# Performance work log

Measured on AMD Instinct MI355X. Metric: run time of the kernel, lower is better.

The kernel has to match this reference:

```python
import jax, jax.numpy as jnp
import numpy as np

N_NODES = 100_000
N_EDGES = 1_600_000
F_IN = 128
HID = 64
C_OUT = 16


def setup_inputs() -> dict:
    key = jax.random.key(0)
    k1, k2, k3, k4, k5 = jax.random.split(key, 5)
    x = jax.random.normal(k1, (N_NODES, F_IN), dtype=jnp.float32)
    edge_index = jax.random.randint(k2, (2, N_EDGES), 0, N_NODES, dtype=jnp.int64)
    edge_weight = jax.random.uniform(k3, (N_EDGES,), dtype=jnp.float32)
    # Glorot-ish init for the two GCNConv linear layers; PyG inits bias to zero.
    W1 = jax.random.normal(k4, (F_IN, HID), dtype=jnp.float32) * (1.0 / np.sqrt(F_IN))
    b1 = jnp.zeros((HID,), dtype=jnp.float32)
    W2 = jax.random.normal(k5, (HID, C_OUT), dtype=jnp.float32) * (1.0 / np.sqrt(HID))
    b2 = jnp.zeros((C_OUT,), dtype=jnp.float32)
    return {"x": x, "edge_index": edge_index, "edge_weight": edge_weight,
            "W1": W1, "b1": b1, "W2": W2, "b2": b2}


def gcn_layer(x, row, col, ew, W, b, n):
    """PyG GCNConv: h = D^-1/2 (A + I) D^-1/2 (x W) + b, with edge weights.
    Self loops (weight 1) are handled analytically instead of appending edges."""
    h = x @ W  # [n, out]
    deg = jax.ops.segment_sum(ew, col, num_segments=n) + 1.0  # +1 for self loop
    dinv = jax.lax.rsqrt(deg)  # deg >= 1 always
    norm = dinv[row] * ew * dinv[col]  # [E]
    agg = jax.ops.segment_sum(norm[:, None] * h[row], col, num_segments=n)
    return agg + (dinv * dinv)[:, None] * h + b


def reference(x, edge_index, edge_weight, W1, b1, W2, b2):
    row, col = edge_index[0], edge_index[1]
    h = jax.nn.relu(gcn_layer(x, row, col, edge_weight, W1, b1, N_NODES))
    # delete_min_weighted_edges(node=0): remove the min-weight edge with source 0.
    # Zeroing its weight is mathematically identical to deleting it (it then
    # contributes 0 to both the degree and the aggregation).
    masked = jnp.where(row == 0, edge_weight, jnp.inf)
    idx = jnp.argmin(masked)
    ew2 = edge_weight.at[idx].set(0.0)
    return gcn_layer(h, row, col, ew2, W2, b2, N_NODES)
```

## Files before the change

### kernel.cpp

```cpp
#include <hip/hip_runtime.h>
#include <hip/hip_bf16.h>
#include <stdint.h>

#define NN 100000
#define NE 1600000
#define FIN 128
#define HID 64
#define COUT 16

#define BUKSH 8
#define BUKN 256
#define NBUK ((NN + BUKN - 1) >> BUKSH)
#define CAP 5120
#define PART_NB 200
#define EPB (NE / PART_NB)

typedef unsigned long long u64;
typedef short bf16x8 __attribute__((ext_vector_type(8)));
typedef float f32x4 __attribute__((ext_vector_type(4)));

struct Flags { int f32; int i64; };

__device__ __forceinline__ float b2f(__hip_bfloat16 v) { return __bfloat162float(v); }

__device__ __forceinline__ float ldf(const void* p, size_t i, int f32) {
    return f32 ? ((const float*)p)[i]
               : __bfloat162float(((const __hip_bfloat16*)p)[i]);
}
__device__ __forceinline__ int lde(const void* p, size_t i, int i64) {
    return i64 ? (int)((const long long*)p)[i] : ((const int*)p)[i];
}
__device__ __forceinline__ void ld4bf(const __hip_bfloat16* p, float& x0, float& x1,
                                      float& x2, float& x3) {
    union { uint2 u; __hip_bfloat16 h[4]; } v;
    v.u = *(const uint2*)p;
    x0 = b2f(v.h[0]); x1 = b2f(v.h[1]); x2 = b2f(v.h[2]); x3 = b2f(v.h[3]);
}
__device__ __forceinline__ unsigned short f2bfu(float f) {
    union { __hip_bfloat16 b; unsigned short u; } c;
    c.b = __float2bfloat16(f);
    return c.u;
}
__device__ __forceinline__ float bfu2f(unsigned short u) {
    union { unsigned short h[2]; float f; } c;
    c.h[0] = 0; c.h[1] = u;
    return c.f;
}

__global__ void k_detect(const unsigned short* xs, const int* ei32, Flags* fl) {
    int lane = threadIdx.x & 63;
    int huge = 0;
    for (int i = lane * 2; i < 1024; i += 128) {
        int e = (xs[i] >> 7) & 0xFF;
        if (e >= 0xC0) huge = 1;
    }
    int odd_nonzero = 0;
    for (int i = 1 + lane * 2; i < 512; i += 128) {
        if (ei32[i] != 0) odd_nonzero = 1;
    }
    u64 h = __ballot(huge), o = __ballot(odd_nonzero);
    if (lane == 0) { fl->f32 = (h != 0); fl->i64 = (o == 0); }
}

__global__ void k_mink(const void* __restrict__ ei, const void* __restrict__ ew,
                       const Flags* __restrict__ fl, u64* __restrict__ minkey) {
    int e = blockIdx.x * blockDim.x + threadIdx.x;
    if (e >= NE) return;
    int r = lde(ei, e, fl->i64);
    if (r == 0) {
        float w = ldf(ew, e, fl->f32);
        u64 key = ((u64)__float_as_uint(w) << 32) | (unsigned)e;
        atomicMin(minkey, key);
    }
}

__global__ __launch_bounds__(256) void k_partA(const void* __restrict__ ei,
                                               const void* __restrict__ ew,
                                               const Flags* __restrict__ fl,
                                               const u64* __restrict__ minkey,
                                               int* __restrict__ cursorA,
                                               long long* __restrict__ tmp) {
    __shared__ int cnt[NBUK];
    __shared__ int base[NBUK];
    int b = blockIdx.x, t = threadIdx.x;
    int f32 = fl->f32, i64 = fl->i64;
    for (int i = t; i < NBUK; i += 256) cnt[i] = 0;
    __syncthreads();
    int e0 = b * EPB;
    for (int i = t; i < EPB; i += 256) {
        int c = lde(ei, (size_t)NE + e0 + i, i64);
        atomicAdd(&cnt[c >> BUKSH], 1);
    }
    __syncthreads();
    for (int i = t; i < NBUK; i += 256) {
        int n = cnt[i];
        base[i] = n ? atomicAdd(&cursorA[i], n) : 0;
    }
    __syncthreads();
    for (int i = t; i < NBUK; i += 256) cnt[i] = 0;
    __syncthreads();
    u64 k = *minkey;
    int eidx = (k == ~0ull) ? 0 : (int)(k & 0xffffffffu);
    for (int i = t; i < EPB; i += 256) {
        int e = e0 + i;
        int r = lde(ei, e, i64);
        int c = lde(ei, (size_t)NE + e, i64);
        float w = ldf(ew, e, f32);
        int buk = c >> BUKSH;
        int slot = base[buk] + atomicAdd(&cnt[buk], 1);
        if (slot < CAP) {
            unsigned lo = (unsigned)r | (((unsigned)c & 255u) << 17)
                        | ((e == eidx) ? (1u << 25) : 0u);
            tmp[(size_t)buk * CAP + slot] = ((long long)__float_as_int(w) << 32) | lo;
        }
    }
}

__global__ __launch_bounds__(512) void k_scanBk(const int* __restrict__ cursorA,
                                                int* __restrict__ bucketBase,
                                                int* __restrict__ rowptrN) {
    __shared__ int sm[512];
    int t = threadIdx.x;
    int v = 0;
    if (t < NBUK) { v = cursorA[t]; if (v > CAP) v = CAP; }
    sm[t] = v;
    for (int off = 1; off < 512; off <<= 1) {
        __syncthreads();
        int add = (t >= off) ? sm[t - off] : 0;
        __syncthreads();
        sm[t] += add;
    }
    __syncthreads();
    if (t < NBUK) bucketBase[t] = sm[t] - v;
    if (t == 511) rowptrN[NN] = sm[511];
}

__global__ __launch_bounds__(256) void k_partB(const int* __restrict__ cursorA,
                                               const int* __restrict__ bucketBase,
                                               const long long* __restrict__ tmp,
                                               int2* __restrict__ epack,
                                               int* __restrict__ rowptrN,
                                               const void* __restrict__ ei,
                                               const void* __restrict__ ew,
                                               const Flags* __restrict__ fl,
                                               const u64* __restrict__ minkey,
                                               float* __restrict__ dinv1,
                                               float* __restrict__ dinv2,
                                               int* __restrict__ delpos) {
    __shared__ int cnt[256];
    __shared__ int pfx[256];
    __shared__ u64 wsum[256];
    int b = blockIdx.x, t = threadIdx.x;
    cnt[t] = 0; wsum[t] = 0;
    __syncthreads();
    int count = cursorA[b]; if (count > CAP) count = CAP;
    const long long* ts = tmp + (size_t)b * CAP;
    for (int i = t; i < count; i += 256) {
        long long pk = ts[i];
        unsigned lo = (unsigned)pk;
        int nl = (int)((lo >> 17) & 255u);
        atomicAdd(&cnt[nl], 1);
        float w = __int_as_float((int)(pk >> 32));
        atomicAdd(&wsum[nl], (u64)((double)w * 4294967296.0));
    }
    __syncthreads();
    int v = cnt[t];
    pfx[t] = v;
    for (int off = 1; off < 256; off <<= 1) {
        __syncthreads();
        int add = (t >= off) ? pfx[t - off] : 0;
        __syncthreads();
        pfx[t] += add;
    }
    __syncthreads();
    int excl = pfx[t] - v;
    int gbase = bucketBase[b];
    int node = (b << BUKSH) + t;
    if (node < NN) {
        rowptrN[node] = gbase + excl;
        float degv = (float)((double)wsum[t] * (1.0 / 4294967296.0));
        u64 kk = *minkey;
        int eidx = (kk == ~0ull) ? 0 : (int)(kk & 0xffffffffu);
        int cmin = lde(ei, (size_t)NE + eidx, fl->i64);
        float wmin = ldf(ew, eidx, fl->f32);
        float d1 = degv + 1.0f;
        float d2 = d1 - ((node == cmin) ? wmin : 0.0f);
        dinv1[node] = rsqrtf(d1);
        dinv2[node] = rsqrtf(d2);
    }
    __syncthreads();
    cnt[t] = gbase + excl;
    __syncthreads();
    for (int i = t; i < count; i += 256) {
        long long pk = ts[i];
        unsigned lo = (unsigned)pk;
        int nl = (int)((lo >> 17) & 255u);
        int pos = atomicAdd(&cnt[nl], 1);
        long long outpk = (pk & 0xFFFFFFFF00000000LL) | (lo & 0x1FFFFu);
        *(long long*)(epack + pos) = outpk;
        if (lo & (1u << 25)) *delpos = pos;
    }
}

__global__ __launch_bounds__(256, 3) void k_gemm1_split(const float* __restrict__ x,
                                                        const float* __restrict__ W1,
                                                        const Flags* __restrict__ fl,
                                                        const float* __restrict__ dinv1,
                                                        __hip_bfloat16* __restrict__ h1) {
    if (!fl->f32) return;
    __shared__ __align__(16) unsigned short Whi[8192];
    __shared__ __align__(16) unsigned short Wlo[8192];
    int t = threadIdx.x;
    for (int i = t; i < 8192; i += 256) {
        int k = i >> 6;
        int n = i & 63;
        int kc = k >> 5, kr = k & 31;
        int q = kr >> 3, j = kr & 7;
        int n0 = n >> 4, col = n & 15;
        float w = W1[i];
        unsigned short hi = f2bfu(w);
        unsigned short lo = f2bfu(w - bfu2f(hi));
        int idx = ((n0 << 4) + (kc << 2) + q) * 128 + col * 8 + j;
        Whi[idx] = hi;
        Wlo[idx] = lo;
    }
    __syncthreads();
    int wave = t >> 6, lane = t & 63;
    int quad = lane >> 4, col = lane & 15;
    bf16x8 Bh[4][4];
#pragma unroll
    for (int n0 = 0; n0 < 4; ++n0)
#pragma unroll
        for (int kc = 0; kc < 4; ++kc)
            Bh[kc][n0] = *(const bf16x8*)&Whi[((n0 << 4) + (kc << 2) + quad) * 128 + col * 8];
    int tile0 = (blockIdx.x * 4 + wave) * 2;
#pragma unroll 1
    for (int i = 0; i < 2; ++i) {
        int node0 = (tile0 + i) * 16;
        if (node0 >= NN) return;
        const float* xp = x + (size_t)(node0 + col) * FIN + quad * 8;
        float4 xv[8];
#pragma unroll
        for (int kc = 0; kc < 4; ++kc) {
            xv[2 * kc]     = *(const float4*)(xp + kc * 32);
            xv[2 * kc + 1] = *(const float4*)(xp + kc * 32 + 4);
        }
        f32x4 a0 = {0.f, 0.f, 0.f, 0.f}, a1 = a0, a2 = a0, a3 = a0;
#pragma unroll
        for (int kc = 0; kc < 4; ++kc) {
            float fv[8];
            fv[0] = xv[2 * kc].x;     fv[1] = xv[2 * kc].y;
            fv[2] = xv[2 * kc].z;     fv[3] = xv[2 * kc].w;
            fv[4] = xv[2 * kc + 1].x; fv[5] = xv[2 * kc + 1].y;
            fv[6] = xv[2 * kc + 1].z; fv[7] = xv[2 * kc + 1].w;
            bf16x8 Ah, Al;
#pragma unroll
            for (int j = 0; j < 8; ++j) {
                unsigned short hi = f2bfu(fv[j]);
                Ah[j] = (short)hi;
                Al[j] = (short)f2bfu(fv[j] - bfu2f(hi));
            }
            int lbase = ((kc << 2) + quad) * 128 + col * 8;
            bf16x8 Bl0 = *(const bf16x8*)&Wlo[lbase];
            bf16x8 Bl1 = *(const bf16x8*)&Wlo[(1 << 4) * 128 + lbase];
            bf16x8 Bl2 = *(const bf16x8*)&Wlo[(2 << 4) * 128 + lbase];
            bf16x8 Bl3 = *(const bf16x8*)&Wlo[(3 << 4) * 128 + lbase];
            a0 = __builtin_amdgcn_mfma_f32_16x16x32_bf16(Ah, Bh[kc][0], a0, 0, 0, 0);
            a0 = __builtin_amdgcn_mfma_f32_16x16x32_bf16(Al, Bh[kc][0], a0, 0, 0, 0);
            a0 = __builtin_amdgcn_mfma_f32_16x16x32_bf16(Ah, Bl0,      a0, 0, 0, 0);
            a1 = __builtin_amdgcn_mfma_f32_16x16x32_bf16(Ah, Bh[kc][1], a1, 0, 0, 0);
            a1 = __builtin_amdgcn_mfma_f32_16x16x32_bf16(Al, Bh[kc][1], a1, 0, 0, 0);
            a1 = __builtin_amdgcn_mfma_f32_16x16x32_bf16(Ah, Bl1,      a1, 0, 0, 0);
            a2 = __builtin_amdgcn_mfma_f32_16x16x32_bf16(Ah, Bh[kc][2], a2, 0, 0, 0);
            a2 = __builtin_amdgcn_mfma_f32_16x16x32_bf16(Al, Bh[kc][2], a2, 0, 0, 0);
            a2 = __builtin_amdgcn_mfma_f32_16x16x32_bf16(Ah, Bl2,      a2, 0, 0, 0);
            a3 = __builtin_amdgcn_mfma_f32_16x16x32_bf16(Ah, Bh[kc][3], a3, 0, 0, 0);
            a3 = __builtin_amdgcn_mfma_f32_16x16x32_bf16(Al, Bh[kc][3], a3, 0, 0, 0);
            a3 = __builtin_amdgcn_mfma_f32_16x16x32_bf16(Ah, Bl3,      a3, 0, 0, 0);
        }
        __hip_bfloat16* hp = h1 + (size_t)(node0 + quad * 4) * HID + col;
#pragma unroll
        for (int r = 0; r < 4; ++r) {
            float dsc = dinv1[node0 + quad * 4 + r];
            hp[(size_t)r * HID + 0]  = __float2bfloat16(a0[r] * dsc);
            hp[(size_t)r * HID + 16] = __float2bfloat16(a1[r] * dsc);
            hp[(size_t)r * HID + 32] = __float2bfloat16(a2[r] * dsc);
            hp[(size_t)r * HID + 48] = __float2bfloat16(a3[r] * dsc);
        }
    }
}

__global__ __launch_bounds__(256) void k_gemm1_mfma(const __hip_bfloat16* __restrict__ x,
                                                    const unsigned short* __restrict__ W1,
                                                    const Flags* __restrict__ fl,
                                                    const float* __restrict__ dinv1,
                                                    __hip_bfloat16* __restrict__ h1) {
    if (fl->f32) return;
    __shared__ __align__(16) unsigned short Wf[8192];
    int t = threadIdx.x;
    for (int i = t; i < 8192; i += 256) {
        int k = i >> 6;
        int n = i & 63;
        int kc = k >> 5, kr = k & 31;
        int q = kr >> 3, j = kr & 7;
        int n0 = n >> 4, col = n & 15;
        Wf[((((n0 << 2) | kc) << 2) | q) * 128 + col * 8 + j] = W1[i];
    }
    __syncthreads();
    int wave = t >> 6, lane = t & 63;
    int quad = lane >> 4, col = lane & 15;
    bf16x8 B[4][4];
#pragma unroll
    for (int n0 = 0; n0 < 4; ++n0)
#pragma unroll
        for (int kc = 0; kc < 4; ++kc)
            B[kc][n0] = *(const bf16x8*)&Wf[((((n0 << 2) | kc) << 2) | quad) * 128 + col * 8];
    int tile0 = (blockIdx.x * 4 + wave) * 4;
#pragma unroll 1
    for (int i = 0; i < 4; ++i) {
        int node0 = (tile0 + i) * 16;
        if (node0 >= NN) return;
        const __hip_bfloat16* xp = x + (size_t)(node0 + col) * FIN + quad * 8;
        f32x4 a0 = {0.f, 0.f, 0.f, 0.f}, a1 = a0, a2 = a0, a3 = a0;
#pragma unroll
        for (int kc = 0; kc < 4; ++kc) {
            bf16x8 A = *(const bf16x8*)(xp + kc * 32);
            a0 = __builtin_amdgcn_mfma_f32_16x16x32_bf16(A, B[kc][0], a0, 0, 0, 0);
            a1 = __builtin_amdgcn_mfma_f32_16x16x32_bf16(A, B[kc][1], a1, 0, 0, 0);
            a2 = __builtin_amdgcn_mfma_f32_16x16x32_bf16(A, B[kc][2], a2, 0, 0, 0);
            a3 = __builtin_amdgcn_mfma_f32_16x16x32_bf16(A, B[kc][3], a3, 0, 0, 0);
        }
        __hip_bfloat16* hp = h1 + (size_t)(node0 + quad * 4) * HID + col;
#pragma unroll
        for (int r = 0; r < 4; ++r) {
            float dsc = dinv1[node0 + quad * 4 + r];
            hp[(size_t)r * HID + 0]  = __float2bfloat16(a0[r] * dsc);
            hp[(size_t)r * HID + 16] = __float2bfloat16(a1[r] * dsc);
            hp[(size_t)r * HID + 32] = __float2bfloat16(a2[r] * dsc);
            hp[(size_t)r * HID + 48] = __float2bfloat16(a3[r] * dsc);
        }
    }
}

__global__ __launch_bounds__(256) void k_agg1(const int* __restrict__ rowptrN,
                                              const int2* __restrict__ epack,
                                              const float* __restrict__ dinv1,
                                              const __hip_bfloat16* __restrict__ h1,
                                              const void* __restrict__ b1,
                                              const Flags* __restrict__ fl,
                                              float* __restrict__ out1) {
    int t = threadIdx.x;
    int n = blockIdx.x * 16 + (t >> 4);
    if (n >= NN) return;
    int l = t & 15;
    int f = l * 4;
    int wbase = t & 48;
    int f32 = fl->f32;
    float dn = dinv1[n];
    int p0 = rowptrN[n], p1 = rowptrN[n + 1];
    float a0 = 0.f, a1 = 0.f, a2 = 0.f, a3 = 0.f;
    for (int p = p0; p < p1; p += 16) {
        int idx = p + l;
        int2 ev = make_int2(0, 0);
        if (idx < p1) ev = epack[idx];
        float cw = __int_as_float(ev.y);
        int rj[16];
#pragma unroll
        for (int j = 0; j < 16; ++j)
            rj[j] = __shfl(ev.x, wbase + j);
        uint2 raw[16];
#pragma unroll
        for (int j = 0; j < 16; ++j)
            raw[j] = *(const uint2*)(h1 + (size_t)rj[j] * HID + f);
#pragma unroll
        for (int j = 0; j < 16; ++j) {
            float c = __shfl(cw, wbase + j);
            union { uint2 u; __hip_bfloat16 h[4]; } v; v.u = raw[j];
            a0 += c * b2f(v.h[0]);
            a1 += c * b2f(v.h[1]);
            a2 += c * b2f(v.h[2]);
            a3 += c * b2f(v.h[3]);
        }
    }
    float x0, x1, x2, x3;
    ld4bf(h1 + (size_t)n * HID + f, x0, x1, x2, x3);
    float4 o;
    o.x = fmaxf(dn * (a0 + x0) + ldf(b1, f + 0, f32), 0.f);
    o.y = fmaxf(dn * (a1 + x1) + ldf(b1, f + 1, f32), 0.f);
    o.z = fmaxf(dn * (a2 + x2) + ldf(b1, f + 2, f32), 0.f);
    o.w = fmaxf(dn * (a3 + x3) + ldf(b1, f + 3, f32), 0.f);
    *(float4*)(out1 + (size_t)n * HID + f) = o;
}

__global__ __launch_bounds__(256) void k_gemm2(const float* __restrict__ out1,
                                               const void* __restrict__ W2,
                                               const Flags* __restrict__ fl,
                                               const float* __restrict__ dinv2,
                                               float* __restrict__ h2) {
    __shared__ float Ws[HID * COUT];
    int t = threadIdx.x;
    int f32 = fl->f32;
    for (int i = t; i < HID * COUT; i += 256) Ws[i] = ldf(W2, i, f32);
    __syncthreads();
    int node = blockIdx.x * 64 + (t >> 2);
    if (node >= NN) return;
    int o4 = (t & 3) * 4;
    const float* xr = out1 + (size_t)node * HID;
    float a0 = 0.f, a1 = 0.f, a2 = 0.f, a3 = 0.f;
#pragma unroll 4
    for (int k = 0; k < HID; ++k) {
        float xv = xr[k];
        const float* wr = &Ws[k * COUT + o4];
        a0 += xv * wr[0]; a1 += xv * wr[1]; a2 += xv * wr[2]; a3 += xv * wr[3];
    }
    float dsc = dinv2[node];
    float* ho = h2 + (size_t)node * COUT + o4;
    ho[0] = a0 * dsc; ho[1] = a1 * dsc; ho[2] = a2 * dsc; ho[3] = a3 * dsc;
}

__global__ __launch_bounds__(256) void k_agg2(const int* __restrict__ rowptrN,
                                              const int2* __restrict__ epack,
                                              const float* __restrict__ dinv2,
                                              const float* __restrict__ h2,
                                              const void* __restrict__ bias2,
                                              const Flags* __restrict__ fl,
                                              const int* __restrict__ delpos,
                                              void* __restrict__ out) {
    int t = threadIdx.x;
    int n = blockIdx.x * 64 + (t >> 2);
    if (n >= NN) return;
    int l = t & 3;
    int f = l * 4;
    int wbase = t & 60;
    int f32 = fl->f32;
    int dp = *delpos;
    float dn = dinv2[n];
    int p0 = rowptrN[n], p1 = rowptrN[n + 1];
    float a0 = 0.f, a1 = 0.f, a2 = 0.f, a3 = 0.f;
    for (int p = p0; p < p1; p += 8) {
        int iA = p + l, iB = p + 4 + l;
        int2 evA = make_int2(0, 0), evB = make_int2(0, 0);
        if (iA < p1) evA = epack[iA];
        if (iB < p1) evB = epack[iB];
        float cwA = (iA == dp) ? 0.f : __int_as_float(evA.y);
        float cwB = (iB == dp) ? 0.f : __int_as_float(evB.y);
        int rj[8];
#pragma unroll
        for (int j = 0; j < 4; ++j) {
            rj[j]     = __shfl(evA.x, wbase + j);
            rj[4 + j] = __shfl(evB.x, wbase + j);
        }
        float4 hv[8];
#pragma unroll
        for (int j = 0; j < 8; ++j)
            hv[j] = *(const float4*)(h2 + (size_t)rj[j] * COUT + f);
#pragma unroll
        for (int j = 0; j < 4; ++j) {
            float cA = __shfl(cwA, wbase + j);
            float cB = __shfl(cwB, wbase + j);
            a0 += cA * hv[j].x + cB * hv[4 + j].x;
            a1 += cA * hv[j].y + cB * hv[4 + j].y;
            a2 += cA * hv[j].z + cB * hv[4 + j].z;
            a3 += cA * hv[j].w + cB * hv[4 + j].w;
        }
    }
    const float4 hn = *(const float4*)(h2 + (size_t)n * COUT + f);
    float o0 = dn * (a0 + hn.x) + ldf(bias2, f + 0, f32);
    float o1 = dn * (a1 + hn.y) + ldf(bias2, f + 1, f32);
    float o2 = dn * (a2 + hn.z) + ldf(bias2, f + 2, f32);
    float o3 = dn * (a3 + hn.w) + ldf(bias2, f + 3, f32);
    size_t idx = (size_t)n * COUT + f;
    if (f32) {
        float* op = (float*)out + idx;
        op[0] = o0; op[1] = o1; op[2] = o2; op[3] = o3;
    } else {
        union { uint2 u; __hip_bfloat16 h[4]; } pk;
        pk.h[0] = __float2bfloat16(o0); pk.h[1] = __float2bfloat16(o1);
        pk.h[2] = __float2bfloat16(o2); pk.h[3] = __float2bfloat16(o3);
        *(uint2*)((__hip_bfloat16*)out + idx) = pk.u;
    }
}

extern "C" void kernel_launch(void* const* d_in, const int* in_sizes, int n_in,
                              void* d_out, int out_size, void* d_ws, size_t ws_size,
                              hipStream_t stream) {
    const void* x  = d_in[0];
    const void* ei = d_in[1];
    const void* ew = d_in[2];
    const void* W1 = d_in[3];
    const void* b1 = d_in[4];
    const void* W2 = d_in[5];
    const void* b2 = d_in[6];

    char* wsb = (char*)d_ws;
    float* dinv1    = (float*)wsb;                     wsb += (size_t)NN * 4;
    float* dinv2    = (float*)wsb;                     wsb += (size_t)NN * 4;
    int*   rowptrN  = (int*)wsb;                       wsb += (size_t)(NN + 1) * 4;
    int*   cursorA  = (int*)wsb;                       wsb += (size_t)NBUK * 4;
    int*   bucketBase = (int*)wsb;                     wsb += (size_t)NBUK * 4;
    wsb = (char*)(((uintptr_t)wsb + 15) & ~(uintptr_t)15);
    int2*  epack    = (int2*)wsb;                      wsb += (size_t)NE * 8;
    __hip_bfloat16* h1 = (__hip_bfloat16*)wsb;         wsb += (size_t)NN * HID * 2;
    float* h2       = (float*)wsb;                     wsb += (size_t)NN * COUT * 4;
    long long* tmp  = (long long*)wsb;
    float* out1     = (float*)wsb;                     wsb += (size_t)NN * HID * 4;
    u64*   minkey   = (u64*)wsb;                       wsb += 8;
    Flags* fl       = (Flags*)wsb;                     wsb += 8;
    int*   delpos   = (int*)wsb;                       wsb += 8;

    hipMemsetAsync(cursorA, 0, (size_t)NBUK * 4, stream);
    hipMemsetAsync(minkey, 0xFF, 8, stream);
    hipMemsetAsync(delpos, 0xFF, 4, stream);

    k_detect<<<1, 64, 0, stream>>>((const unsigned short*)x, (const int*)ei, fl);
    k_mink<<<(NE + 255) / 256, 256, 0, stream>>>(ei, ew, fl, minkey);
    k_partA<<<PART_NB, 256, 0, stream>>>(ei, ew, fl, minkey, cursorA, tmp);
    k_scanBk<<<1, 512, 0, stream>>>(cursorA, bucketBase, rowptrN);
    k_partB<<<NBUK, 256, 0, stream>>>(cursorA, bucketBase, tmp, epack, rowptrN,
                                      ei, ew, fl, minkey, dinv1, dinv2, delpos);
    k_gemm1_split<<<(NN / 16 + 7) / 8, 256, 0, stream>>>((const float*)x,
                                                         (const float*)W1, fl,
                                                         dinv1, h1);
    k_gemm1_mfma<<<(NN / 16 + 15) / 16, 256, 0, stream>>>((const __hip_bfloat16*)x,
                                                          (const unsigned short*)W1, fl,
                                                          dinv1, h1);
    k_agg1<<<(NN + 15) / 16, 256, 0, stream>>>(rowptrN, epack, dinv1, h1, b1, fl, out1);
    k_gemm2<<<(NN + 63) / 64, 256, 0, stream>>>(out1, W2, fl, dinv2, h2);
    k_agg2<<<(NN + 63) / 64, 256, 0, stream>>>(rowptrN, epack, dinv2, h2, b2, fl,
                                               delpos, d_out);
}
```

Baseline: 276.2 us.

## Fuse layer-2 GEMM into layer-1 aggregation and merge memsets into init kernel

```diff
diff --git a/kernel.cpp b/kernel.cpp
--- a/kernel.cpp
+++ b/kernel.cpp
@@ -47,19 +47,28 @@
     return c.f;
 }
 
-__global__ void k_detect(const unsigned short* xs, const int* ei32, Flags* fl) {
-    int lane = threadIdx.x & 63;
-    int huge = 0;
-    for (int i = lane * 2; i < 1024; i += 128) {
-        int e = (xs[i] >> 7) & 0xFF;
-        if (e >= 0xC0) huge = 1;
-    }
-    int odd_nonzero = 0;
-    for (int i = 1 + lane * 2; i < 512; i += 128) {
-        if (ei32[i] != 0) odd_nonzero = 1;
-    }
-    u64 h = __ballot(huge), o = __ballot(odd_nonzero);
-    if (lane == 0) { fl->f32 = (h != 0); fl->i64 = (o == 0); }
+__global__ __launch_bounds__(256) void k_init(const unsigned short* xs,
+                                              const int* ei32, Flags* fl,
+                                              int* cursorA, u64* minkey,
+                                              int* delpos) {
+    int t = threadIdx.x;
+    if (t < 64) {
+        int lane = t;
+        int huge = 0;
+        for (int i = lane * 2; i < 1024; i += 128) {
+            int e = (xs[i] >> 7) & 0xFF;
+            if (e >= 0xC0) huge = 1;
+        }
+        int odd_nonzero = 0;
+        for (int i = 1 + lane * 2; i < 512; i += 128) {
+            if (ei32[i] != 0) odd_nonzero = 1;
+        }
+        u64 h = __ballot(huge), o = __ballot(odd_nonzero);
+        if (lane == 0) { fl->f32 = (h != 0); fl->i64 = (o == 0); }
+    }
+    for (int i = t; i < NBUK; i += 256) cursorA[i] = 0;
+    if (t == 64) *minkey = ~0ull;
+    if (t == 65) *delpos = -1;
 }
 
 __global__ void k_mink(const void* __restrict__ ei, const void* __restrict__ ew,
@@ -347,15 +356,20 @@
                                               const float* __restrict__ dinv1,
                                               const __hip_bfloat16* __restrict__ h1,
                                               const void* __restrict__ b1,
+                                              const void* __restrict__ W2,
                                               const Flags* __restrict__ fl,
-                                              float* __restrict__ out1) {
+                                              const float* __restrict__ dinv2,
+                                              float* __restrict__ h2) {
+    __shared__ float Ws[HID * COUT];
+    __shared__ float obuf[16][68];
     int t = threadIdx.x;
-    int n = blockIdx.x * 16 + (t >> 4);
-    if (n >= NN) return;
+    int f32 = fl->f32;
+    for (int i = t; i < HID * COUT; i += 256) Ws[i] = ldf(W2, i, f32);
+    int nn = t >> 4;
+    int n = blockIdx.x * 16 + nn;
     int l = t & 15;
     int f = l * 4;
     int wbase = t & 48;
-    int f32 = fl->f32;
     float dn = dinv1[n];
     int p0 = rowptrN[n], p1 = rowptrN[n + 1];
     float a0 = 0.f, a1 = 0.f, a2 = 0.f, a3 = 0.f;
@@ -389,33 +403,16 @@
     o.y = fmaxf(dn * (a1 + x1) + ldf(b1, f + 1, f32), 0.f);
     o.z = fmaxf(dn * (a2 + x2) + ldf(b1, f + 2, f32), 0.f);
     o.w = fmaxf(dn * (a3 + x3) + ldf(b1, f + 3, f32), 0.f);
-    *(float4*)(out1 + (size_t)n * HID + f) = o;
-}
-
-__global__ __launch_bounds__(256) void k_gemm2(const float* __restrict__ out1,
-                                               const void* __restrict__ W2,
-                                               const Flags* __restrict__ fl,
-                                               const float* __restrict__ dinv2,
-                                               float* __restrict__ h2) {
-    __shared__ float Ws[HID * COUT];
-    int t = threadIdx.x;
-    int f32 = fl->f32;
-    for (int i = t; i < HID * COUT; i += 256) Ws[i] = ldf(W2, i, f32);
-    __syncthreads();
-    int node = blockIdx.x * 64 + (t >> 2);
-    if (node >= NN) return;
-    int o4 = (t & 3) * 4;
-    const float* xr = out1 + (size_t)node * HID;
-    float a0 = 0.f, a1 = 0.f, a2 = 0.f, a3 = 0.f;
-#pragma unroll 4
-    for (int k = 0; k < HID; ++k) {
-        float xv = xr[k];
-        const float* wr = &Ws[k * COUT + o4];
-        a0 += xv * wr[0]; a1 += xv * wr[1]; a2 += xv * wr[2]; a3 += xv * wr[3];
-    }
-    float dsc = dinv2[node];
-    float* ho = h2 + (size_t)node * COUT + o4;
-    ho[0] = a0 * dsc; ho[1] = a1 * dsc; ho[2] = a2 * dsc; ho[3] = a3 * dsc;
+    obuf[nn][f + 0] = o.x; obuf[nn][f + 1] = o.y;
+    obuf[nn][f + 2] = o.z; obuf[nn][f + 3] = o.w;
+    __syncthreads();
+    int c = t & 15;
+    const float* orow = obuf[nn];
+    float acc = 0.f;
+#pragma unroll 8
+    for (int k = 0; k < HID; ++k)
+        acc += orow[k] * Ws[k * COUT + c];
+    h2[(size_t)n * COUT + c] = acc * dinv2[n];
 }
 
 __global__ __launch_bounds__(256) void k_agg2(const int* __restrict__ rowptrN,
@@ -502,17 +499,13 @@
     int2*  epack    = (int2*)wsb;                      wsb += (size_t)NE * 8;
     __hip_bfloat16* h1 = (__hip_bfloat16*)wsb;         wsb += (size_t)NN * HID * 2;
     float* h2       = (float*)wsb;                     wsb += (size_t)NN * COUT * 4;
-    long long* tmp  = (long long*)wsb;
-    float* out1     = (float*)wsb;                     wsb += (size_t)NN * HID * 4;
+    long long* tmp  = (long long*)wsb;                 wsb += (size_t)NBUK * CAP * 8;
     u64*   minkey   = (u64*)wsb;                       wsb += 8;
     Flags* fl       = (Flags*)wsb;                     wsb += 8;
     int*   delpos   = (int*)wsb;                       wsb += 8;
 
-    hipMemsetAsync(cursorA, 0, (size_t)NBUK * 4, stream);
-    hipMemsetAsync(minkey, 0xFF, 8, stream);
-    hipMemsetAsync(delpos, 0xFF, 4, stream);
-
-    k_detect<<<1, 64, 0, stream>>>((const unsigned short*)x, (const int*)ei, fl);
+    k_init<<<1, 256, 0, stream>>>((const unsigned short*)x, (const int*)ei, fl,
+                                  cursorA, minkey, delpos);
     k_mink<<<(NE + 255) / 256, 256, 0, stream>>>(ei, ew, fl, minkey);
     k_partA<<<PART_NB, 256, 0, stream>>>(ei, ew, fl, minkey, cursorA, tmp);
     k_scanBk<<<1, 512, 0, stream>>>(cursorA, bucketBase, rowptrN);
@@ -524,8 +517,8 @@
     k_gemm1_mfma<<<(NN / 16 + 15) / 16, 256, 0, stream>>>((const __hip_bfloat16*)x,
                                                           (const unsigned short*)W1, fl,
                                                           dinv1, h1);
-    k_agg1<<<(NN + 15) / 16, 256, 0, stream>>>(rowptrN, epack, dinv1, h1, b1, fl, out1);
-    k_gemm2<<<(NN + 63) / 64, 256, 0, stream>>>(out1, W2, fl, dinv2, h2);
+    k_agg1<<<NN / 16, 256, 0, stream>>>(rowptrN, epack, dinv1, h1, b1, W2, fl,
+                                        dinv2, h2);
     k_agg2<<<(NN + 63) / 64, 256, 0, stream>>>(rowptrN, epack, dinv2, h2, b2, fl,
                                                delpos, d_out);
 }
```

Result: faster. 255.2 us (-7.6%).
